# Performance work log

Measured on AMD Instinct MI355X. Metric: run time of the kernel, lower is better.

## Reference

```python
import jax, jax.numpy as jnp
import numpy as np

# ---- SLAYER neuron / simulation params (netParams) ----
THETA = 10.0      # spike threshold
TAU_SR = 10.0     # PSP (SRM alpha) time constant
TAU_REF = 1.0     # refractory time constant
TAU_RHO = 1.0     # surrogate-gradient width factor (pdfTimeConstant = tauRho*theta)
SCALE_RHO = 1.0
TS = 1.0
T_SAMPLE = 300

def _alpha_kernel(tau, mult, eps=0.01):
    # replicates slayer._calculateAlphaKernel: truncated alpha kernel
    vals = []
    for t in np.arange(0.0, T_SAMPLE, TS):
        v = mult * t / tau * np.exp(1.0 - t / tau)
        if abs(v) < eps and t > tau:
            break
        vals.append(v)
    return jnp.asarray(np.array(vals, np.float32))

SRM = _alpha_kernel(TAU_SR, 1.0)              # ~77-tap causal PSP filter
REF = _alpha_kernel(TAU_REF, -2.0 * THETA)    # short refractory kernel (REF[0]=0)


def psp(x):
    """Causal FIR filter along last (time) axis: y[t] = sum_s x[t-s]*SRM[s]."""
    K = SRM.shape[0]
    sh = x.shape
    T = sh[-1]
    xr = x.reshape(-1, 1, T)                 # (M, 1, T)
    w = SRM[::-1].reshape(1, 1, K)           # reversed for cross-correlation
    y = jax.lax.conv_general_dilated(xr, w, (1,), [(K - 1, 0)])
    return y.reshape(sh)


def _spike_scan(u):
    """LIF/SRM spike generation with refractory feedback (slayerCuda.getSpikes).
    Returns (spikes, effective membrane potential incl. refractory)."""
    sh = u.shape
    T = sh[-1]
    uf = u.reshape(-1, T).T                  # (T, M)
    K = REF.shape[0]
    M = uf.shape[1]

    def step(buf, ut):
        # buf[k] = refractory contribution to membrane at time t+k from past spikes
        ueff = ut + buf[0]
        s = (ueff >= THETA).astype(ut.dtype)  # spike value 1/Ts with Ts=1
        buf = buf + s[None, :] * REF[:, None]  # REF[0]=0, so current step unaffected
        buf = jnp.concatenate([buf[1:], jnp.zeros((1, M), ut.dtype)], axis=0)
        return buf, (s, ueff)

    _, (S, U) = jax.lax.scan(step, jnp.zeros((K, M), u.dtype), uf)
    return S.T.reshape(sh), U.T.reshape(sh)


@jax.custom_vjp
def spike(u):
    return _spike_scan(u)[0]

def _spike_fwd(u):
    s, ueff = _spike_scan(u)
    return s, ueff

def _spike_bwd(ueff, g):
    # SLAYER surrogate gradient: pdfScale/pdfTimeConstant * exp(-|u - theta|/pdfTimeConstant)
    tc = TAU_RHO * THETA
    return (g * (SCALE_RHO / tc) * jnp.exp(-jnp.abs(ueff - THETA) / tc),)

spike.defvjp(_spike_fwd, _spike_bwd)


def conv3(x, w, pad):
    # spatial conv per time step: x (N,C,H,W,T), w (O,I,kh,kw,1)
    dn = jax.lax.conv_dimension_numbers(x.shape, w.shape, ('NCHWT', 'OIHWT', 'NCHWT'))
    return jax.lax.conv_general_dilated(
        x, w, (1, 1, 1), [(pad, pad), (pad, pad), (0, 0)], dimension_numbers=dn)


def pool2(x):
    # slayer pool: 2x2 sum-pool per channel, fixed weight 1.1*theta/(k*k)
    N, C, H, W, T = x.shape
    return x.reshape(N, C, H // 2, 2, W // 2, 2, T).sum(axis=(3, 5)) * (1.1 * THETA / 4.0)


def dense(x, w):
    # slayer dense((8,8,64),10): full-spatial conv == linear over (C,H,W) per time step
    y = jnp.einsum('nchwt,ochw->not', x, w)
    return y[:, :, None, None, :]             # (N,10,1,1,T)


def _forward(x, w1, w2, w3, wfc):
    s1 = spike(conv3(psp(x), w1, 1))          # (N,16,32,32,T)
    s2 = spike(pool2(psp(s1)))                # (N,16,16,16,T)
    s3 = spike(conv3(psp(s2), w2, 1))         # (N,32,16,16,T)
    s4 = spike(pool2(psp(s3)))                # (N,32,8,8,T)
    s5 = spike(conv3(psp(s4), w3, 1))         # (N,64,8,8,T)
    return spike(dense(psp(s5), wfc))         # (N,10,1,1,T)


def setup_inputs() -> dict:
    key = jax.random.key(0)
    k = jax.random.split(key, 5)
    x = (jax.random.uniform(k[0], (8, 2, 34, 34, 300)) < 0.05).astype(jnp.float32)
    w1 = jax.random.normal(k[1], (16, 2, 5, 5, 1), jnp.float32) * 0.5
    w2 = jax.random.normal(k[2], (32, 16, 3, 3, 1), jnp.float32) * 0.2
    w3 = jax.random.normal(k[3], (64, 32, 3, 3, 1), jnp.float32) * 0.15
    wfc = jax.random.normal(k[4], (10, 64, 8, 8), jnp.float32) * 0.05
    return {"spikeInput": x, "w1": w1, "w2": w2, "w3": w3, "wfc": wfc}


def reference(spikeInput, w1, w2, w3, wfc):
    return _forward(spikeInput, w1, w2, w3, wfc)
```

## Files before the change

### kernel.cpp

```cpp
#include <hip/hip_runtime.h>
#include <cmath>

#define THETA 10.0f

__device__ __forceinline__ void init_srm(float* srm) {
    int tid = threadIdx.x;
    if (tid < 77) {
        double td = (double)tid;
        srm[tid] = (float)(td / 10.0 * exp(1.0 - td / 10.0));
    }
    __syncthreads();
}

__global__ void transpose_kernel(const float* __restrict__ in, float* __restrict__ out,
                                 int M, int T) {
    __shared__ float tile[32][33];
    int mBase = blockIdx.x * 32;
    int tBase = blockIdx.y * 32;
    int tx = threadIdx.x, ty = threadIdx.y;
    for (int i = ty; i < 32; i += 8) {
        int m = mBase + i, t = tBase + tx;
        if (m < M && t < T) tile[i][tx] = in[(size_t)m * T + t];
    }
    __syncthreads();
    for (int i = ty; i < 32; i += 8) {
        int t = tBase + i, m = mBase + tx;
        if (t < T && m < M) out[(size_t)t * M + m] = tile[tx][i];
    }
}

template <int TT>
__global__ void psp_kernel(const float* __restrict__ in, float* __restrict__ out,
                           int M) {
    __shared__ float srm_s[77];
    init_srm(srm_s);
    int tb = blockIdx.y * TT;
    int m = blockIdx.x * blockDim.x + threadIdx.x;
    if (m >= M) return;
    float c[77];
#pragma unroll
    for (int s = 0; s < 77; ++s) c[s] = srm_s[s];
    float acc[TT];
#pragma unroll
    for (int j = 0; j < TT; ++j) acc[j] = 0.f;
#pragma unroll
    for (int k = TT - 1; k >= 0; --k) {
        float v = in[(size_t)(tb + k) * M + m];
#pragma unroll
        for (int j = k; j < TT; ++j) acc[j] = fmaf(v, c[j - k], acc[j]);
    }
#pragma unroll
    for (int s0 = 1; s0 <= 77 - TT; ++s0) {
        int u = tb - s0;
        if (u >= 0) {
            float v = in[(size_t)u * M + m];
#pragma unroll
            for (int j = 0; j < TT; ++j) acc[j] = fmaf(v, c[s0 + j], acc[j]);
        }
    }
#pragma unroll
    for (int k = 78 - TT; k <= 76; ++k) {
        int u = tb - k;
        if (u >= 0) {
            float v = in[(size_t)u * M + m];
#pragma unroll
            for (int j = 0; j <= 76 - k; ++j) acc[j] = fmaf(v, c[k + j], acc[j]);
        }
    }
#pragma unroll
    for (int j = 0; j < TT; ++j) out[(size_t)(tb + j) * M + m] = acc[j];
}

template <int TT>
__global__ void psppool_kernel(const float* __restrict__ in, float* __restrict__ out,
                               int NC, int Hin, int Win) {
    __shared__ float srm_s[77];
    init_srm(srm_s);
    int Ho = Hin >> 1, Wo = Win >> 1;
    int Mout = NC * Ho * Wo;
    int Min = NC * Hin * Win;
    int tb = blockIdx.y * TT;
    int mo = blockIdx.x * blockDim.x + threadIdx.x;
    if (mo >= Mout) return;
    int X = mo % Wo;
    int Y = (mo / Wo) % Ho;
    int nc = mo / (Wo * Ho);
    int base = nc * Hin * Win + (2 * Y) * Win + 2 * X;
    float c[77];
#pragma unroll
    for (int s = 0; s < 77; ++s) c[s] = srm_s[s];
    float acc[TT];
#pragma unroll
    for (int j = 0; j < TT; ++j) acc[j] = 0.f;
#pragma unroll
    for (int k = TT - 1; k >= 0; --k) {
        const float* p = in + (size_t)(tb + k) * Min + base;
        float v = (p[0] + p[1]) + (p[Win] + p[Win + 1]);
#pragma unroll
        for (int j = k; j < TT; ++j) acc[j] = fmaf(c[j - k], v, acc[j]);
    }
#pragma unroll
    for (int s0 = 1; s0 <= 77 - TT; ++s0) {
        int u = tb - s0;
        if (u >= 0) {
            const float* p = in + (size_t)u * Min + base;
            float v = (p[0] + p[1]) + (p[Win] + p[Win + 1]);
#pragma unroll
            for (int j = 0; j < TT; ++j) acc[j] = fmaf(c[s0 + j], v, acc[j]);
        }
    }
#pragma unroll
    for (int k = 78 - TT; k <= 76; ++k) {
        int u = tb - k;
        if (u >= 0) {
            const float* p = in + (size_t)u * Min + base;
            float v = (p[0] + p[1]) + (p[Win] + p[Win + 1]);
#pragma unroll
            for (int j = 0; j <= 76 - k; ++j) acc[j] = fmaf(c[k + j], v, acc[j]);
        }
    }
#pragma unroll
    for (int j = 0; j < TT; ++j)
        out[(size_t)(tb + j) * Mout + mo] = acc[j] * 2.75f;
}

__global__ __launch_bounds__(256) void conv1_v4(const float* __restrict__ in,
                                                const float* __restrict__ w,
                                                float* __restrict__ out) {
    __shared__ float s_in[2592];
    __shared__ float s_w[800];
    int n = blockIdx.x, t = blockIdx.y, tid = threadIdx.x;
    const float* src = in + ((size_t)t * 8 + n) * 2312;
    for (int idx = tid; idx < 2592; idx += 256) {
        int ch = idx / 1296, rem = idx % 1296;
        int r = rem / 36, col = rem % 36;
        float v = 0.f;
        if (r >= 1 && r <= 34 && col >= 1 && col <= 34)
            v = src[ch * 1156 + (r - 1) * 34 + (col - 1)];
        s_in[idx] = v;
    }
    for (int idx = tid; idx < 800; idx += 256) {
        int tap = idx >> 4, o = idx & 15;
        s_w[tap * 16 + o] = w[o * 50 + tap];
    }
    __syncthreads();
    int x = tid & 31, y0 = tid >> 5;
    float acc[4][16];
#pragma unroll
    for (int q = 0; q < 4; ++q)
#pragma unroll
        for (int o = 0; o < 16; ++o) acc[q][o] = 0.f;
#pragma unroll
    for (int i = 0; i < 2; ++i) {
#pragma unroll
        for (int ky = 0; ky < 5; ++ky) {
#pragma unroll
            for (int kx = 0; kx < 5; ++kx) {
                int tap = i * 25 + ky * 5 + kx;
                float v[4];
#pragma unroll
                for (int q = 0; q < 4; ++q)
                    v[q] = s_in[i * 1296 + (y0 + 8 * q + ky) * 36 + (x + kx)];
                const float4* wp = (const float4*)&s_w[tap * 16];
#pragma unroll
                for (int oq = 0; oq < 4; ++oq) {
                    float4 w4 = wp[oq];
#pragma unroll
                    for (int q = 0; q < 4; ++q) {
                        acc[q][oq * 4 + 0] = fmaf(v[q], w4.x, acc[q][oq * 4 + 0]);
                        acc[q][oq * 4 + 1] = fmaf(v[q], w4.y, acc[q][oq * 4 + 1]);
                        acc[q][oq * 4 + 2] = fmaf(v[q], w4.z, acc[q][oq * 4 + 2]);
                        acc[q][oq * 4 + 3] = fmaf(v[q], w4.w, acc[q][oq * 4 + 3]);
                    }
                }
            }
        }
    }
    float* dst = out + ((size_t)t * 8 + n) * 16384;
#pragma unroll
    for (int q = 0; q < 4; ++q) {
        int y = y0 + 8 * q;
#pragma unroll
        for (int o = 0; o < 16; ++o) dst[o * 1024 + y * 32 + x] = acc[q][o];
    }
}

__global__ __launch_bounds__(256) void conv2_v3(const float* __restrict__ in,
                                                const float* __restrict__ w,
                                                float* __restrict__ out) {
    __shared__ float s_in[5184];
    int n = blockIdx.x, t = blockIdx.y, ob = blockIdx.z * 16;
    int tid = threadIdx.x;
    const float* src = in + ((size_t)t * 8 + n) * 4096;
    for (int idx = tid; idx < 5184; idx += 256) {
        int c = idx / 324, rem = idx % 324;
        int r = rem / 18, col = rem % 18;
        float v = 0.f;
        if (r >= 1 && r <= 16 && col >= 1 && col <= 16)
            v = src[c * 256 + (r - 1) * 16 + (col - 1)];
        s_in[idx] = v;
    }
    __syncthreads();
    int x = tid & 15, y = tid >> 4;
    float acc[16];
#pragma unroll
    for (int o = 0; o < 16; ++o) acc[o] = 0.f;
    for (int i = 0; i < 16; ++i) {
        const float* base = &s_in[i * 324 + y * 18 + x];
        float vv[9];
#pragma unroll
        for (int ky = 0; ky < 3; ++ky)
#pragma unroll
            for (int kx = 0; kx < 3; ++kx) vv[ky * 3 + kx] = base[ky * 18 + kx];
#pragma unroll
        for (int tap = 0; tap < 9; ++tap) {
            float v = vv[tap];
            const float* wp = w + (size_t)ob * 144 + i * 9 + tap;
#pragma unroll
            for (int o = 0; o < 16; ++o)
                acc[o] = fmaf(v, wp[o * 144], acc[o]);
        }
    }
    float* dst = out + (((size_t)t * 8 + n) * 32 + ob) * 256;
#pragma unroll
    for (int o = 0; o < 16; ++o) dst[o * 256 + tid] = acc[o];
}

__global__ __launch_bounds__(256) void conv3_v3(const float* __restrict__ in,
                                                const float* __restrict__ w,
                                                float* __restrict__ out) {
    __shared__ float s_in[8192];
    int n0 = blockIdx.x * 4, t = blockIdx.y, ob = blockIdx.z * 16;
    int tid = threadIdx.x;
    const float* src = in + ((size_t)t * 16384 + n0 * 2048);
    for (int i = tid; i < 8192; i += 256) s_in[i] = src[i];
    __syncthreads();
    int ln = tid >> 6;
    int pos = tid & 63;
    int y = pos >> 3, x = pos & 7;
    bool mask[9];
    int off[9];
#pragma unroll
    for (int ky = 0; ky < 3; ++ky) {
        int iy = y + ky - 1;
        bool ry = (unsigned)iy < 8u;
#pragma unroll
        for (int kx = 0; kx < 3; ++kx) {
            int ix = x + kx - 1;
            bool ok = ry && ((unsigned)ix < 8u);
            mask[ky * 3 + kx] = ok;
            off[ky * 3 + kx] = ok ? (iy * 8 + ix) : 0;
        }
    }
    const float* base = &s_in[ln * 2048];
    float acc[16];
#pragma unroll
    for (int o = 0; o < 16; ++o) acc[o] = 0.f;
    for (int i = 0; i < 32; ++i) {
        const float* ip = base + i * 64;
        float vv[9];
#pragma unroll
        for (int tap = 0; tap < 9; ++tap)
            vv[tap] = mask[tap] ? ip[off[tap]] : 0.f;
#pragma unroll
        for (int tap = 0; tap < 9; ++tap) {
            float v = vv[tap];
            const float* wp = w + (size_t)ob * 288 + i * 9 + tap;
#pragma unroll
            for (int o = 0; o < 16; ++o)
                acc[o] = fmaf(v, wp[o * 288], acc[o]);
        }
    }
    float* dst = out + (((size_t)t * 8 + n0 + ln) * 64 + ob) * 64;
#pragma unroll
    for (int o = 0; o < 16; ++o) dst[o * 64 + pos] = acc[o];
}

template <int CH>
__global__ void spike_kernel(float* __restrict__ u, int M, int T) {
    int m = blockIdx.x * blockDim.x + threadIdx.x;
    if (m >= M) return;
    float ref[11];
#pragma unroll
    for (int k = 0; k < 11; ++k)
        ref[k] = (float)(-20.0 * (double)k * exp(1.0 - (double)k));
    float r[11];
#pragma unroll
    for (int k = 0; k < 11; ++k) r[k] = 0.f;
    float a[CH], b[CH];
#pragma unroll
    for (int j = 0; j < CH; ++j) a[j] = u[(size_t)j * M + m];
    int NC = T / CH;
    for (int c = 0; c < NC; ++c) {
        if (c + 1 < NC) {
#pragma unroll
            for (int j = 0; j < CH; ++j)
                b[j] = u[(size_t)((c + 1) * CH + j) * M + m];
        }
#pragma unroll
        for (int j = 0; j < CH; ++j) {
            float ue = a[j] + r[0];
            float s = (ue >= THETA) ? 1.0f : 0.0f;
            u[(size_t)(c * CH + j) * M + m] = s;
#pragma unroll
            for (int k = 0; k < 10; ++k) r[k] = fmaf(s, ref[k + 1], r[k + 1]);
        }
#pragma unroll
        for (int j = 0; j < CH; ++j) a[j] = b[j];
    }
}

__global__ void dense_kernel(const float* __restrict__ p, const float* __restrict__ wfc,
                             float* __restrict__ out) {
    int n = blockIdx.x;
    int t = blockIdx.y;
    int tid = threadIdx.x;
    const float* row = p + ((size_t)t * 8 + n) * 4096;
    float acc[10];
#pragma unroll
    for (int o = 0; o < 10; ++o) acc[o] = 0.f;
    for (int j = tid; j < 4096; j += 256) {
        float v = row[j];
#pragma unroll
        for (int o = 0; o < 10; ++o) acc[o] = fmaf(v, wfc[o * 4096 + j], acc[o]);
    }
    __shared__ float red[4][10];
#pragma unroll
    for (int o = 0; o < 10; ++o) {
        float a = acc[o];
        for (int off = 32; off > 0; off >>= 1) a += __shfl_down(a, off, 64);
        acc[o] = a;
    }
    int wave = tid >> 6, lane = tid & 63;
    if (lane == 0) {
#pragma unroll
        for (int o = 0; o < 10; ++o) red[wave][o] = acc[o];
    }
    __syncthreads();
    if (tid < 10) {
        float a = (red[0][tid] + red[1][tid]) + (red[2][tid] + red[3][tid]);
        out[((size_t)t * 8 + n) * 10 + tid] = a;
    }
}

template <int CH>
__global__ void spike_out_kernel(const float* __restrict__ u, float* __restrict__ out,
                                 int M, int T) {
    int m = blockIdx.x * blockDim.x + threadIdx.x;
    if (m >= M) return;
    float ref[11];
#pragma unroll
    for (int k = 0; k < 11; ++k)
        ref[k] = (float)(-20.0 * (double)k * exp(1.0 - (double)k));
    float r[11];
#pragma unroll
    for (int k = 0; k < 11; ++k) r[k] = 0.f;
    float a[CH], b[CH];
#pragma unroll
    for (int j = 0; j < CH; ++j) a[j] = u[(size_t)j * M + m];
    int NC = T / CH;
    for (int c = 0; c < NC; ++c) {
        if (c + 1 < NC) {
#pragma unroll
            for (int j = 0; j < CH; ++j)
                b[j] = u[(size_t)((c + 1) * CH + j) * M + m];
        }
#pragma unroll
        for (int j = 0; j < CH; ++j) {
            float ue = a[j] + r[0];
            float s = (ue >= THETA) ? 1.0f : 0.0f;
            out[(size_t)m * T + c * CH + j] = s;
#pragma unroll
            for (int k = 0; k < 10; ++k) r[k] = fmaf(s, ref[k + 1], r[k + 1]);
        }
#pragma unroll
        for (int j = 0; j < CH; ++j) a[j] = b[j];
    }
}

extern "C" void kernel_launch(void* const* d_in, const int* in_sizes, int n_in,
                              void* d_out, int out_size, void* d_ws, size_t ws_size,
                              hipStream_t stream) {
    const float* x   = (const float*)d_in[0];
    const float* w1  = (const float*)d_in[1];
    const float* w2  = (const float*)d_in[2];
    const float* w3  = (const float*)d_in[3];
    const float* wfc = (const float*)d_in[4];
    float* outp = (float*)d_out;

    float* slotB = (float*)d_ws;
    float* slotA = slotB + 39321600;
    const int T = 300;
    dim3 blk(256);
    dim3 blk64(64);
    constexpr int TT = 20;
    constexpr int CH = 10;

    transpose_kernel<<<dim3(578, 10), dim3(32, 8), 0, stream>>>(x, slotB, 18496, T);
    psp_kernel<TT><<<dim3(73, 15), blk, 0, stream>>>(slotB, slotA, 18496);
    conv1_v4<<<dim3(8, T), blk, 0, stream>>>(slotA, w1, slotB);
    spike_kernel<CH><<<dim3(2048), blk64, 0, stream>>>(slotB, 131072, T);
    psppool_kernel<TT><<<dim3(128, 15), blk, 0, stream>>>(slotB, slotA, 8 * 16, 32, 32);
    spike_kernel<CH><<<dim3(512), blk64, 0, stream>>>(slotA, 32768, T);
    psp_kernel<TT><<<dim3(128, 15), blk, 0, stream>>>(slotA, slotB, 32768);
    conv2_v3<<<dim3(8, T, 2), blk, 0, stream>>>(slotB, w2, slotA);
    spike_kernel<CH><<<dim3(1024), blk64, 0, stream>>>(slotA, 65536, T);
    psppool_kernel<TT><<<dim3(64, 15), blk, 0, stream>>>(slotA, slotB, 8 * 32, 16, 16);
    spike_kernel<CH><<<dim3(256), blk64, 0, stream>>>(slotB, 16384, T);
    psp_kernel<TT><<<dim3(64, 15), blk, 0, stream>>>(slotB, slotA, 16384);
    conv3_v3<<<dim3(2, T, 4), blk, 0, stream>>>(slotA, w3, slotB);
    spike_kernel<CH><<<dim3(512), blk64, 0, stream>>>(slotB, 32768, T);
    psp_kernel<TT><<<dim3(128, 15), blk, 0, stream>>>(slotB, slotA, 32768);
    dense_kernel<<<dim3(8, T), blk, 0, stream>>>(slotA, wfc, slotB);
    spike_out_kernel<CH><<<dim3(2), dim3(64), 0, stream>>>(slotB, outp, 80, T);
}
```

Before: 965.0 us.

## Store intermediate spike trains as uint8 and read them in PSP kernels

```diff
diff --git a/kernel.cpp b/kernel.cpp
--- a/kernel.cpp
+++ b/kernel.cpp
@@ -72,8 +72,51 @@
 }
 
 template <int TT>
-__global__ void psppool_kernel(const float* __restrict__ in, float* __restrict__ out,
-                               int NC, int Hin, int Win) {
+__global__ void psp_u8_kernel(const unsigned char* __restrict__ in,
+                              float* __restrict__ out, int M) {
+    __shared__ float srm_s[77];
+    init_srm(srm_s);
+    int tb = blockIdx.y * TT;
+    int m = blockIdx.x * blockDim.x + threadIdx.x;
+    if (m >= M) return;
+    float c[77];
+#pragma unroll
+    for (int s = 0; s < 77; ++s) c[s] = srm_s[s];
+    float acc[TT];
+#pragma unroll
+    for (int j = 0; j < TT; ++j) acc[j] = 0.f;
+#pragma unroll
+    for (int k = TT - 1; k >= 0; --k) {
+        float v = (float)in[(size_t)(tb + k) * M + m];
+#pragma unroll
+        for (int j = k; j < TT; ++j) acc[j] = fmaf(v, c[j - k], acc[j]);
+    }
+#pragma unroll
+    for (int s0 = 1; s0 <= 77 - TT; ++s0) {
+        int u = tb - s0;
+        if (u >= 0) {
+            float v = (float)in[(size_t)u * M + m];
+#pragma unroll
+            for (int j = 0; j < TT; ++j) acc[j] = fmaf(v, c[s0 + j], acc[j]);
+        }
+    }
+#pragma unroll
+    for (int k = 78 - TT; k <= 76; ++k) {
+        int u = tb - k;
+        if (u >= 0) {
+            float v = (float)in[(size_t)u * M + m];
+#pragma unroll
+            for (int j = 0; j <= 76 - k; ++j) acc[j] = fmaf(v, c[k + j], acc[j]);
+        }
+    }
+#pragma unroll
+    for (int j = 0; j < TT; ++j) out[(size_t)(tb + j) * M + m] = acc[j];
+}
+
+template <int TT>
+__global__ void psppool_u8_kernel(const unsigned char* __restrict__ in,
+                                  float* __restrict__ out,
+                                  int NC, int Hin, int Win) {
     __shared__ float srm_s[77];
     init_srm(srm_s);
     int Ho = Hin >> 1, Wo = Win >> 1;
@@ -94,8 +137,10 @@
     for (int j = 0; j < TT; ++j) acc[j] = 0.f;
 #pragma unroll
     for (int k = TT - 1; k >= 0; --k) {
-        const float* p = in + (size_t)(tb + k) * Min + base;
-        float v = (p[0] + p[1]) + (p[Win] + p[Win + 1]);
+        const unsigned char* p = in + (size_t)(tb + k) * Min + base;
+        uchar2 a0 = *reinterpret_cast<const uchar2*>(p);
+        uchar2 a1 = *reinterpret_cast<const uchar2*>(p + Win);
+        float v = (float)((int)a0.x + (int)a0.y + (int)a1.x + (int)a1.y);
 #pragma unroll
         for (int j = k; j < TT; ++j) acc[j] = fmaf(c[j - k], v, acc[j]);
     }
@@ -103,8 +148,10 @@
     for (int s0 = 1; s0 <= 77 - TT; ++s0) {
         int u = tb - s0;
         if (u >= 0) {
-            const float* p = in + (size_t)u * Min + base;
-            float v = (p[0] + p[1]) + (p[Win] + p[Win + 1]);
+            const unsigned char* p = in + (size_t)u * Min + base;
+            uchar2 a0 = *reinterpret_cast<const uchar2*>(p);
+            uchar2 a1 = *reinterpret_cast<const uchar2*>(p + Win);
+            float v = (float)((int)a0.x + (int)a0.y + (int)a1.x + (int)a1.y);
 #pragma unroll
             for (int j = 0; j < TT; ++j) acc[j] = fmaf(c[s0 + j], v, acc[j]);
         }
@@ -113,8 +160,10 @@
     for (int k = 78 - TT; k <= 76; ++k) {
         int u = tb - k;
         if (u >= 0) {
-            const float* p = in + (size_t)u * Min + base;
-            float v = (p[0] + p[1]) + (p[Win] + p[Win + 1]);
+            const unsigned char* p = in + (size_t)u * Min + base;
+            uchar2 a0 = *reinterpret_cast<const uchar2*>(p);
+            uchar2 a1 = *reinterpret_cast<const uchar2*>(p + Win);
+            float v = (float)((int)a0.x + (int)a0.y + (int)a1.x + (int)a1.y);
 #pragma unroll
             for (int j = 0; j <= 76 - k; ++j) acc[j] = fmaf(c[k + j], v, acc[j]);
         }
@@ -277,7 +326,8 @@
 }
 
 template <int CH>
-__global__ void spike_kernel(float* __restrict__ u, int M, int T) {
+__global__ void spike_u8_kernel(const float* __restrict__ u,
+                                unsigned char* __restrict__ sp, int M, int T) {
     int m = blockIdx.x * blockDim.x + threadIdx.x;
     if (m >= M) return;
     float ref[11];
@@ -301,7 +351,7 @@
         for (int j = 0; j < CH; ++j) {
             float ue = a[j] + r[0];
             float s = (ue >= THETA) ? 1.0f : 0.0f;
-            u[(size_t)(c * CH + j) * M + m] = s;
+            sp[(size_t)(c * CH + j) * M + m] = (unsigned char)(ue >= THETA);
 #pragma unroll
             for (int k = 0; k < 10; ++k) r[k] = fmaf(s, ref[k + 1], r[k + 1]);
         }
@@ -390,6 +440,9 @@
 
     float* slotB = (float*)d_ws;
     float* slotA = slotB + 39321600;
+    unsigned char* s1_u8 = (unsigned char*)(slotA + 9830400);
+    unsigned char* sB_u8 = (unsigned char*)(slotB + 9830400);
+    unsigned char* s5_u8 = (unsigned char*)slotA;
     const int T = 300;
     dim3 blk(256);
     dim3 blk64(64);
@@ -399,18 +452,19 @@
     transpose_kernel<<<dim3(578, 10), dim3(32, 8), 0, stream>>>(x, slotB, 18496, T);
     psp_kernel<TT><<<dim3(73, 15), blk, 0, stream>>>(slotB, slotA, 18496);
     conv1_v4<<<dim3(8, T), blk, 0, stream>>>(slotA, w1, slotB);
-    spike_kernel<CH><<<dim3(2048), blk64, 0, stream>>>(slotB, 131072, T);
-    psppool_kernel<TT><<<dim3(128, 15), blk, 0, stream>>>(slotB, slotA, 8 * 16, 32, 32);
-    spike_kernel<CH><<<dim3(512), blk64, 0, stream>>>(slotA, 32768, T);
-    psp_kernel<TT><<<dim3(128, 15), blk, 0, stream>>>(slotA, slotB, 32768);
+    spike_u8_kernel<CH><<<dim3(2048), blk64, 0, stream>>>(slotB, s1_u8, 131072, T);
+    psppool_u8_kernel<TT><<<dim3(128, 15), blk, 0, stream>>>(s1_u8, slotA, 8 * 16, 32, 32);
+    spike_u8_kernel<CH><<<dim3(512), blk64, 0, stream>>>(slotA, sB_u8, 32768, T);
+    psp_u8_kernel<TT><<<dim3(128, 15), blk, 0, stream>>>(sB_u8, slotB, 32768);
     conv2_v3<<<dim3(8, T, 2), blk, 0, stream>>>(slotB, w2, slotA);
-    spike_kernel<CH><<<dim3(1024), blk64, 0, stream>>>(slotA, 65536, T);
-    psppool_kernel<TT><<<dim3(64, 15), blk, 0, stream>>>(slotA, slotB, 8 * 32, 16, 16);
-    spike_kernel<CH><<<dim3(256), blk64, 0, stream>>>(slotB, 16384, T);
-    psp_kernel<TT><<<dim3(64, 15), blk, 0, stream>>>(slotB, slotA, 16384);
+    spike_u8_kernel<CH><<<dim3(1024), blk64, 0, stream>>>(slotA, sB_u8, 65536, T);
+    psppool_u8_kernel<TT><<<dim3(64, 15), blk, 0, stream>>>(sB_u8, slotB, 8 * 32, 16, 16);
+    spike_u8_kernel<CH><<<dim3(256), blk64, 0, stream>>>(slotB, sB_u8, 16384, T);
+    psp_u8_kernel<TT><<<dim3(64, 15), blk, 0, stream>>>(sB_u8, slotA, 16384);
     conv3_v3<<<dim3(2, T, 4), blk, 0, stream>>>(slotA, w3, slotB);
-    spike_kernel<CH><<<dim3(512), blk64, 0, stream>>>(slotB, 32768, T);
-    psp_kernel<TT><<<dim3(128, 15), blk, 0, stream>>>(slotB, slotA, 32768);
-    dense_kernel<<<dim3(8, T), blk, 0, stream>>>(slotA, wfc, slotB);
-    spike_out_kernel<CH><<<dim3(2), dim3(64), 0, stream>>>(slotB, outp, 80, T);
-}
+    spike_u8_kernel<CH><<<dim3(512), blk64, 0, stream>>>(slotB, s5_u8, 32768, T);
+    psp_u8_kernel<TT><<<dim3(128, 15), blk, 0, stream>>>(s5_u8, slotB, 32768);
+    float* u6 = slotA + 16000000;
+    dense_kernel<<<dim3(8, T), blk, 0, stream>>>(slotB, wfc, u6);
+    spike_out_kernel<CH><<<dim3(2), dim3(64), 0, stream>>>(u6, outp, 80, T);
+}
```

Result: faster. 830.2 us (-14.0%).
